# Kernel tuning notes

Hardware: AMD Instinct MI355X
Metric: run time of the kernel (lower is better)

The kernel has to match this reference:

```python
import jax, jax.numpy as jnp
import numpy as np

START_TAG = 30
END_TAG = 31
INVALID = -10000.0  # Constants.Invalid_Transition


def setup_inputs() -> dict:
    key = jax.random.key(0)
    k1, k2, k3, k4 = jax.random.split(key, 4)
    B, T, K = 1024, 512, 32
    feats = jax.random.normal(k1, (B, T, K), dtype=jnp.float32)
    tags = jax.random.randint(k2, (B, T), 0, START_TAG)  # gold tags exclude START/END
    lengths = jax.random.randint(k3, (B,), 1, T + 1)
    sentence_masks = (jnp.arange(T)[None, :] < lengths[:, None]).astype(jnp.int32)
    transitions = jax.random.normal(k4, (K, K), dtype=jnp.float32) * 0.1
    # transitions[i, j] = score of transitioning from tag j to tag i
    transitions = transitions.at[START_TAG, :].set(INVALID).at[:, END_TAG].set(INVALID)
    return {"feats": feats, "transitions": transitions, "tags": tags,
            "sentence_masks": sentence_masks}


def _gold_score(feats, transitions, tags, sentence_masks):
    # Faithful port of _score_sentence
    B, T, K = feats.shape
    emit = jnp.take_along_axis(feats, tags[:, :, None], axis=2)[:, :, 0]  # [B,T]
    emit = emit * sentence_masks.astype(feats.dtype)
    pad_start = jnp.concatenate([jnp.full((B, 1), START_TAG, tags.dtype), tags], axis=1)
    pad_end = jnp.concatenate([tags, jnp.full((B, 1), END_TAG, tags.dtype)], axis=1)
    trans = transitions[pad_end, pad_start]  # [B,T+1]
    tmask = jnp.concatenate([jnp.ones((B, 1), sentence_masks.dtype), sentence_masks], axis=1)
    trans = trans * tmask.astype(feats.dtype)
    return jnp.sum(emit, axis=1) + jnp.sum(trans, axis=1)  # [B]


def _log_partition(feats, transitions, sentence_masks):
    # Faithful port of _forward_alg: sequential DP over time, logsumexp over prev tags
    B, T, K = feats.shape
    lengths = jnp.sum(sentence_masks, axis=1)  # [B]
    init = jnp.full((K,), INVALID, dtype=feats.dtype).at[START_TAG].set(0.0)
    init = jnp.broadcast_to(init, (B, K))

    def step(forward_var, feat):
        # tag_var[b, next, prev] = alpha[b, prev] + trans[next, prev] + emit[b, next]
        tag_var = forward_var[:, None, :] + transitions[None, :, :] + feat[:, :, None]
        new = jax.nn.logsumexp(tag_var, axis=2)  # [B,K]
        return new, new

    _, all_alphas = jax.lax.scan(step, init, jnp.swapaxes(feats, 0, 1))  # [T,B,K]
    idx = jnp.broadcast_to((lengths - 1)[None, :, None], (1, B, K))
    last_alpha = jnp.take_along_axis(all_alphas, idx, axis=0)[0]  # [B,K]
    terminal = last_alpha + transitions[END_TAG][None, :]
    return jax.nn.logsumexp(terminal, axis=1)  # [B]


def reference(feats, transitions, tags, sentence_masks):
    # CRF negative log-likelihood per sentence: Z - gold_score
    Z = _log_partition(feats, transitions, sentence_masks)
    gold = _gold_score(feats, transitions, tags, sentence_masks)
    return Z - gold  # [B]
```

## Files before the change

### kernel.cpp

```cpp
#include <hip/hip_runtime.h>

#define KT 32
#define START_TAG 30
#define END_TAG 31

__device__ __forceinline__ float exp2f_fast(float x){ return __builtin_amdgcn_exp2f(x); }
__device__ __forceinline__ float log2f_fast(float x){ return __builtin_amdgcn_logf(x); }
__device__ __forceinline__ float readlane_f(float v, int l){
    return __int_as_float(__builtin_amdgcn_readlane(__float_as_int(v), l));
}

__global__ __launch_bounds__(128, 2) void crf_nll(
    const float* __restrict__ feats,
    const float* __restrict__ trans,
    const int*   __restrict__ tags,
    const int*   __restrict__ masks,
    float* __restrict__ out, int B, int T)
{
    constexpr float L2E = 1.4426950408889634f;
    constexpr float LN2 = 0.6931471805599453f;
    const int tid  = (int)threadIdx.x;
    const int lane = tid & 63;
    const int wid  = tid >> 6;
    const int k    = lane & 31;
    const int b    = (int)blockIdx.x;

    __shared__ float Tl[KT * KT];
    __shared__ __align__(16) float ftile[2][2][32][KT];
    __shared__ float cvec[KT];
    __shared__ int   cMF;

    for (int i = tid; i < KT * KT; i += 128) Tl[i] = trans[i];

    float E[KT];
    float E2 = 0.f;
    if (wid == 0) {
#pragma unroll
        for (int j = 0; j < KT; ++j) E[j] = exp2f_fast(trans[k * KT + j] * L2E);
    } else {
#pragma unroll
        for (int m = 0; m < KT; ++m) E[m] = exp2f_fast(trans[m * KT + k] * L2E);
        E2 = exp2f_fast(trans[END_TAG * KT + k] * L2E);
    }
    __syncthreads();

    const float4* f4 = (const float4*)(feats + (size_t)b * T * KT);
    const int*    mk = masks + (size_t)b * T;
    const int*    tg = tags  + (size_t)b * T;
    const float*  fb = feats + (size_t)b * T * KT;

    int Lp = 0;
    for (int c = 0; c < T; c += 64) { const int t = c + lane; if (t < T) Lp += mk[t]; }
#pragma unroll
    for (int d = 1; d < 64; d <<= 1) Lp += __shfl_xor(Lp, d);
    const int L   = Lp;
    const int mf  = (L + 1) >> 1;
    const int ntT = T >> 5;

    float4 R0, R1, R2, R3, S0, S1, S2, S3;
    float y = 0.f, Fc = 0.f, f1 = 0.f, f2 = 0.f, g = 0.f;
    int   M = 0;

#define TLOADR(ti_) { const int o=(ti_)*256+lane; R0=f4[o];R1=f4[o+64];R2=f4[o+128];R3=f4[o+192]; }
#define TLOADS(ti_) { const int o=(ti_)*256+lane; S0=f4[o];S1=f4[o+64];S2=f4[o+128];S3=f4[o+192]; }
#define TWRITER(bf) { float4* w=(float4*)&ftile[wid][bf][0][0]; w[lane]=R0;w[lane+64]=R1;w[lane+128]=R2;w[lane+192]=R3; }
#define TWRITES(bf) { float4* w=(float4*)&ftile[wid][bf][0][0]; w[lane]=S0;w[lane+64]=S1;w[lane+128]=S2;w[lane+192]=S3; }
#define FEAT(t_) ftile[wid][((t_)>>5)&1][(t_)&31][k]

    if (wid == 0) {
        TLOADR(0)
        if (ntT > 1) TLOADS(1)
        TWRITER(0)
        if (ntT > 1) TWRITES(1)
        y  = (k == START_TAG) ? 1.f : 0.f;
        Fc = exp2f_fast(FEAT(0) * L2E);
        f1 = FEAT(1);
        f2 = FEAT(2);
        const int ntA = (mf + 31) >> 5;
        for (int n = 0; n < ntA; ++n) {
            for (int c = 0; c < 4; ++c) {
#pragma unroll
                for (int u = 0; u < 8; ++u) {
                    const int ti_ = c * 8 + u;
                    const int t   = (n << 5) + ti_;
                    if (ti_ == 0)  { const int nx = n + 2; if (nx < ntA) TLOADR(nx) }
                    float sv[32];
#pragma unroll
                    for (int j = 0; j < 32; ++j) sv[j] = readlane_f(y, j);
                    __builtin_amdgcn_sched_barrier(0);
                    const unsigned pb = __float_as_uint(sv[0]);
                    int e = (int)((pb >> 23) & 255u);
                    if (e < 1 || e > 253) e = 127;
                    const float Fcr = Fc * __uint_as_float((unsigned)(254 - e) << 23);
                    float a0 = 0.f, a1 = 0.f, a2 = 0.f, a3 = 0.f;
#pragma unroll
                    for (int j = 0; j < 32; j += 4) {
                        a0 = fmaf(E[j+0], sv[j+0], a0);
                        a1 = fmaf(E[j+1], sv[j+1], a1);
                        a2 = fmaf(E[j+2], sv[j+2], a2);
                        a3 = fmaf(E[j+3], sv[j+3], a3);
                    }
                    const float val = ((a0 + a1) + (a2 + a3)) * Fcr;
                    const bool act = t < mf;
                    y  = act ? val : y;
                    M += act ? (e - 127) : 0;
                    if (ti_ == 30) { const int nx = n + 2; if (nx < ntA) TWRITER((n & 1)) }
                    const float fnew = FEAT(t + 3);
                    Fc = exp2f_fast(f1 * L2E);
                    f1 = f2; f2 = fnew;
                }
            }
        }
        if (lane < 32) cvec[k] = y;
        if (tid == 0) cMF = M;
    } else {
        const int n_hi = (L - 1) >> 5;
        const int n_lo = mf >> 5;
        TLOADR(n_hi)
        if (n_hi >= 1) TLOADS(n_hi - 1)
        float4 Q0, Q1, Q2, Q3;
        if (n_hi >= 2) { const int o=(n_hi-2)*256+lane; Q0=f4[o];Q1=f4[o+64];Q2=f4[o+128];Q3=f4[o+192]; }

        for (int c = 0; c < T; c += 64) {
            const int t = c + lane;
            if (t < T) {
                const int mt    = mk[t];
                const int tagt  = tg[t];
                const int prev  = t ? tg[t - 1] : START_TAG;
                const int fprev = t ? mk[t - 1] : 1;
                if (mt)    g += fb[(size_t)t * KT + tagt];
                if (fprev) g += Tl[tagt * KT + prev];
                if (t == T - 1 && mt) g += Tl[END_TAG * KT + tagt];
            }
        }
#pragma unroll
        for (int d = 1; d < 64; d <<= 1) g += __shfl_xor(g, d);

        TWRITER((n_hi & 1))
        if (n_hi >= 1) TWRITES(((n_hi - 1) & 1))
        y = E2; M = 0;
        Fc = exp2f_fast(FEAT(L - 1) * L2E);
        f1 = FEAT(L - 2);
        f2 = FEAT(L - 3);

#define BSTEP(T_, DO_LD, LD_TI, DO_WR, WR_BF) {                               \
        if (DO_LD) TLOADR(LD_TI)                                              \
        const float bb = y * Fc;                                              \
        float sv[32];                                                         \
        _Pragma("unroll")                                                     \
        for (int j = 0; j < 32; ++j) sv[j] = readlane_f(bb, j);               \
        __builtin_amdgcn_sched_barrier(0);                                    \
        const unsigned pb = __float_as_uint(sv[0]);                           \
        int e = (int)((pb >> 23) & 255u);                                     \
        if (e < 1 || e > 253) e = 127;                                        \
        const float r = __uint_as_float((unsigned)(254 - e) << 23);           \
        float a0 = 0.f, a1 = 0.f, a2 = 0.f, a3 = 0.f;                         \
        _Pragma("unroll")                                                     \
        for (int j = 0; j < 32; j += 4) {                                     \
            a0 = fmaf(E[j+0], sv[j+0], a0);                                   \
            a1 = fmaf(E[j+1], sv[j+1], a1);                                   \
            a2 = fmaf(E[j+2], sv[j+2], a2);                                   \
            a3 = fmaf(E[j+3], sv[j+3], a3);                                   \
        }                                                                     \
        const float val = ((a0 + a1) + (a2 + a3)) * r;                        \
        const bool act = (T_) >= mf;                                          \
        y  = act ? val : y;                                                   \
        M += act ? (e - 127) : 0;                                             \
        if (DO_WR) TWRITER(WR_BF)                                             \
        const float fnew = FEAT((T_) - 3);                                    \
        Fc = exp2f_fast(f1 * L2E);                                            \
        f1 = f2; f2 = fnew; }

        for (int t = L - 1; t >= (n_hi << 5); --t) {
            BSTEP(t, false, 0, false, 0)
        }
        if (n_hi >= 2) { float4* w=(float4*)&ftile[wid][(n_hi & 1)][0][0];
                         w[lane]=Q0;w[lane+64]=Q1;w[lane+128]=Q2;w[lane+192]=Q3; }
        for (int n = n_hi - 1; n >= n_lo; --n) {
            for (int c = 0; c < 4; ++c) {
#pragma unroll
                for (int u = 0; u < 8; ++u) {
                    const int ti_ = c * 8 + u;
                    const int t   = (n << 5) + 31 - ti_;
                    BSTEP(t, (ti_ == 0) && (n >= n_lo + 2), n - 2,
                             (ti_ == 29) && (n >= n_lo + 2), (n & 1))
                }
            }
        }
#undef BSTEP
    }

    __syncthreads();
    if (wid == 1) {
        float term = y * cvec[k];
#pragma unroll
        for (int d = 1; d < 32; d <<= 1) term += __shfl_xor(term, d);
        const float Z = ((float)(M + cMF) + log2f_fast(term)) * LN2;
        if (lane == 0) out[b] = Z - g;
    }
#undef TLOADR
#undef TLOADS
#undef TWRITER
#undef TWRITES
#undef FEAT
}

extern "C" void kernel_launch(void* const* d_in, const int* in_sizes, int n_in,
                              void* d_out, int out_size, void* d_ws, size_t ws_size,
                              hipStream_t stream) {
    const float* feats = (const float*)d_in[0];
    const float* trans = (const float*)d_in[1];
    const int*   tags  = (const int*)d_in[2];
    const int*   masks = (const int*)d_in[3];
    float* out = (float*)d_out;

    const int B = out_size;
    const int T = in_sizes[2] / B;

    hipLaunchKernelGGL(crf_nll, dim3(B), dim3(128), 0, stream,
                       feats, trans, tags, masks, out, B, T);
}
```

Measured before the change: 167.9 us.

## Split CRF matvec across wave halves using ds_swizzle broadcast

Each 32-lane half of the wavefront now handles 16 of the 32 previous tags, so a lane holds 16 transition exponentials instead of 32. The broadcasts use ds_swizzle in place of 32 serial readlanes, and the two partial sums are combined with a cross-half shuffle. The renormalization exponent is read with readfirstlane from the new state and applied at the next step, which takes the scale computation off the critical path. Swizzle and shuffle go through the LDS crossbar, which may add latency to each sequential step in place of the scalar readlane path.

New measurement: 152.8 us. -9.0%, faster.

```diff
diff --git a/kernel.cpp b/kernel.cpp
--- a/kernel.cpp
+++ b/kernel.cpp
@@ -6,9 +6,8 @@
 
 __device__ __forceinline__ float exp2f_fast(float x){ return __builtin_amdgcn_exp2f(x); }
 __device__ __forceinline__ float log2f_fast(float x){ return __builtin_amdgcn_logf(x); }
-__device__ __forceinline__ float readlane_f(float v, int l){
-    return __int_as_float(__builtin_amdgcn_readlane(__float_as_int(v), l));
-}
+
+#define SWZB(v, J) __int_as_float(__builtin_amdgcn_ds_swizzle(__float_as_int(v), ((J) << 5)))
 
 __global__ __launch_bounds__(128, 2) void crf_nll(
     const float* __restrict__ feats,
@@ -22,7 +21,9 @@
     const int tid  = (int)threadIdx.x;
     const int lane = tid & 63;
     const int wid  = tid >> 6;
-    const int k    = lane & 31;
+    const int li   = lane & 31;
+    const int h    = lane >> 5;
+    const int ok   = (li + (h << 4)) & 31;
     const int b    = (int)blockIdx.x;
 
     __shared__ float Tl[KT * KT];
@@ -32,15 +33,15 @@
 
     for (int i = tid; i < KT * KT; i += 128) Tl[i] = trans[i];
 
-    float E[KT];
-    float E2 = 0.f;
+    float Eh[16];
     if (wid == 0) {
 #pragma unroll
-        for (int j = 0; j < KT; ++j) E[j] = exp2f_fast(trans[k * KT + j] * L2E);
+        for (int j = 0; j < 16; ++j)
+            Eh[j] = exp2f_fast(trans[ok * KT + (h << 4) + j] * L2E);
     } else {
 #pragma unroll
-        for (int m = 0; m < KT; ++m) E[m] = exp2f_fast(trans[m * KT + k] * L2E);
-        E2 = exp2f_fast(trans[END_TAG * KT + k] * L2E);
+        for (int j = 0; j < 16; ++j)
+            Eh[j] = exp2f_fast(trans[((h << 4) + j) * KT + ok] * L2E);
     }
     __syncthreads();
 
@@ -53,30 +54,50 @@
     for (int c = 0; c < T; c += 64) { const int t = c + lane; if (t < T) Lp += mk[t]; }
 #pragma unroll
     for (int d = 1; d < 64; d <<= 1) Lp += __shfl_xor(Lp, d);
-    const int L   = Lp;
-    const int mf  = (L + 1) >> 1;
-    const int ntT = T >> 5;
+    const int L  = Lp;
+    const int mf = (L + 1) >> 1;
 
     float4 R0, R1, R2, R3, S0, S1, S2, S3;
-    float y = 0.f, Fc = 0.f, f1 = 0.f, f2 = 0.f, g = 0.f;
-    int   M = 0;
+    float y = 0.f, Fcr = 0.f, f1 = 0.f, f2 = 0.f, g = 0.f;
+    int   M = 0, dMp = 0;
 
 #define TLOADR(ti_) { const int o=(ti_)*256+lane; R0=f4[o];R1=f4[o+64];R2=f4[o+128];R3=f4[o+192]; }
 #define TLOADS(ti_) { const int o=(ti_)*256+lane; S0=f4[o];S1=f4[o+64];S2=f4[o+128];S3=f4[o+192]; }
 #define TWRITER(bf) { float4* w=(float4*)&ftile[wid][bf][0][0]; w[lane]=R0;w[lane+64]=R1;w[lane+128]=R2;w[lane+192]=R3; }
 #define TWRITES(bf) { float4* w=(float4*)&ftile[wid][bf][0][0]; w[lane]=S0;w[lane+64]=S1;w[lane+128]=S2;w[lane+192]=S3; }
-#define FEAT(t_) ftile[wid][((t_)>>5)&1][(t_)&31][k]
+#define FEAT(t_) ftile[wid][((t_)>>5)&1][(t_)&31][ok]
+
+#define MATVEC(SRC, SS)                                                        \
+    const float b0=SWZB(SRC,0),  b1=SWZB(SRC,1),  b2=SWZB(SRC,2),  b3=SWZB(SRC,3),  \
+                b4=SWZB(SRC,4),  b5=SWZB(SRC,5),  b6=SWZB(SRC,6),  b7=SWZB(SRC,7),  \
+                b8=SWZB(SRC,8),  b9=SWZB(SRC,9),  b10=SWZB(SRC,10),b11=SWZB(SRC,11),\
+                b12=SWZB(SRC,12),b13=SWZB(SRC,13),b14=SWZB(SRC,14),b15=SWZB(SRC,15);\
+    float a0 = Eh[0]*b0, a1 = Eh[1]*b1, a2 = Eh[2]*b2, a3 = Eh[3]*b3;          \
+    a0 = fmaf(Eh[4], b4, a0);  a1 = fmaf(Eh[5], b5, a1);                       \
+    a2 = fmaf(Eh[6], b6, a2);  a3 = fmaf(Eh[7], b7, a3);                       \
+    a0 = fmaf(Eh[8], b8, a0);  a1 = fmaf(Eh[9], b9, a1);                       \
+    a2 = fmaf(Eh[10],b10,a2);  a3 = fmaf(Eh[11],b11,a3);                       \
+    a0 = fmaf(Eh[12],b12,a0);  a1 = fmaf(Eh[13],b13,a1);                       \
+    a2 = fmaf(Eh[14],b14,a2);  a3 = fmaf(Eh[15],b15,a3);                       \
+    const float pp = (a0 + a1) + (a2 + a3);                                    \
+    const float SS = pp + __shfl_xor(pp, 48);
+
+#define CAPTURE(SS)                                                            \
+    { const int cap = __builtin_amdgcn_readfirstlane(__float_as_int(SS));      \
+      int e = (cap >> 23) & 255; if (e < 1 || e > 253) e = 127;                \
+      dMp = e - 127;                                                           \
+      Fcr = exp2f_fast(f1 * L2E) * __uint_as_float((unsigned)(254 - e) << 23); }
 
     if (wid == 0) {
+        const int ntA = (mf + 31) >> 5;
         TLOADR(0)
-        if (ntT > 1) TLOADS(1)
+        if (ntA > 1) TLOADS(1)
         TWRITER(0)
-        if (ntT > 1) TWRITES(1)
-        y  = (k == START_TAG) ? 1.f : 0.f;
-        Fc = exp2f_fast(FEAT(0) * L2E);
-        f1 = FEAT(1);
-        f2 = FEAT(2);
-        const int ntA = (mf + 31) >> 5;
+        if (ntA > 1) TWRITES(1)
+        y   = (ok == START_TAG) ? 1.f : 0.f;
+        Fcr = exp2f_fast(FEAT(0) * L2E);
+        f1  = FEAT(1);
+        f2  = FEAT(2);
         for (int n = 0; n < ntA; ++n) {
             for (int c = 0; c < 4; ++c) {
 #pragma unroll
@@ -84,35 +105,20 @@
                     const int ti_ = c * 8 + u;
                     const int t   = (n << 5) + ti_;
                     if (ti_ == 0)  { const int nx = n + 2; if (nx < ntA) TLOADR(nx) }
-                    float sv[32];
-#pragma unroll
-                    for (int j = 0; j < 32; ++j) sv[j] = readlane_f(y, j);
-                    __builtin_amdgcn_sched_barrier(0);
-                    const unsigned pb = __float_as_uint(sv[0]);
-                    int e = (int)((pb >> 23) & 255u);
-                    if (e < 1 || e > 253) e = 127;
-                    const float Fcr = Fc * __uint_as_float((unsigned)(254 - e) << 23);
-                    float a0 = 0.f, a1 = 0.f, a2 = 0.f, a3 = 0.f;
-#pragma unroll
-                    for (int j = 0; j < 32; j += 4) {
-                        a0 = fmaf(E[j+0], sv[j+0], a0);
-                        a1 = fmaf(E[j+1], sv[j+1], a1);
-                        a2 = fmaf(E[j+2], sv[j+2], a2);
-                        a3 = fmaf(E[j+3], sv[j+3], a3);
-                    }
-                    const float val = ((a0 + a1) + (a2 + a3)) * Fcr;
-                    const bool act = t < mf;
+                    const float fnew = FEAT(t + 3);
+                    MATVEC(y, ss)
+                    const float val = ss * Fcr;
+                    const bool  act = t < mf;
                     y  = act ? val : y;
-                    M += act ? (e - 127) : 0;
+                    M += act ? dMp : 0;
+                    CAPTURE(ss)
                     if (ti_ == 30) { const int nx = n + 2; if (nx < ntA) TWRITER((n & 1)) }
-                    const float fnew = FEAT(t + 3);
-                    Fc = exp2f_fast(f1 * L2E);
                     f1 = f2; f2 = fnew;
                 }
             }
         }
-        if (lane < 32) cvec[k] = y;
-        if (tid == 0) cMF = M;
+        if (lane < 32) cvec[lane] = y;
+        if (tid == 0)  cMF = M;
     } else {
         const int n_hi = (L - 1) >> 5;
         const int n_lo = mf >> 5;
@@ -138,37 +144,21 @@
 
         TWRITER((n_hi & 1))
         if (n_hi >= 1) TWRITES(((n_hi - 1) & 1))
-        y = E2; M = 0;
-        Fc = exp2f_fast(FEAT(L - 1) * L2E);
-        f1 = FEAT(L - 2);
-        f2 = FEAT(L - 3);
+        y   = exp2f_fast(trans[END_TAG * KT + ok] * L2E);
+        Fcr = exp2f_fast(FEAT(L - 1) * L2E);
+        f1  = FEAT(L - 2);
+        f2  = FEAT(L - 3);
 
 #define BSTEP(T_, DO_LD, LD_TI, DO_WR, WR_BF) {                               \
         if (DO_LD) TLOADR(LD_TI)                                              \
-        const float bb = y * Fc;                                              \
-        float sv[32];                                                         \
-        _Pragma("unroll")                                                     \
-        for (int j = 0; j < 32; ++j) sv[j] = readlane_f(bb, j);               \
-        __builtin_amdgcn_sched_barrier(0);                                    \
-        const unsigned pb = __float_as_uint(sv[0]);                           \
-        int e = (int)((pb >> 23) & 255u);                                     \
-        if (e < 1 || e > 253) e = 127;                                        \
-        const float r = __uint_as_float((unsigned)(254 - e) << 23);           \
-        float a0 = 0.f, a1 = 0.f, a2 = 0.f, a3 = 0.f;                         \
-        _Pragma("unroll")                                                     \
-        for (int j = 0; j < 32; j += 4) {                                     \
-            a0 = fmaf(E[j+0], sv[j+0], a0);                                   \
-            a1 = fmaf(E[j+1], sv[j+1], a1);                                   \
-            a2 = fmaf(E[j+2], sv[j+2], a2);                                   \
-            a3 = fmaf(E[j+3], sv[j+3], a3);                                   \
-        }                                                                     \
-        const float val = ((a0 + a1) + (a2 + a3)) * r;                        \
+        const float fnew = FEAT((T_) - 3);                                    \
+        const float bb = y * Fcr;                                             \
+        MATVEC(bb, ss)                                                        \
         const bool act = (T_) >= mf;                                          \
-        y  = act ? val : y;                                                   \
-        M += act ? (e - 127) : 0;                                             \
+        y  = act ? ss : y;                                                    \
+        M += act ? dMp : 0;                                                   \
+        CAPTURE(ss)                                                           \
         if (DO_WR) TWRITER(WR_BF)                                             \
-        const float fnew = FEAT((T_) - 3);                                    \
-        Fc = exp2f_fast(f1 * L2E);                                            \
         f1 = f2; f2 = fnew; }
 
         for (int t = L - 1; t >= (n_hi << 5); --t) {
@@ -192,10 +182,10 @@
 
     __syncthreads();
     if (wid == 1) {
-        float term = y * cvec[k];
-#pragma unroll
-        for (int d = 1; d < 32; d <<= 1) term += __shfl_xor(term, d);
-        const float Z = ((float)(M + cMF) + log2f_fast(term)) * LN2;
+        float term = y * cvec[ok];
+#pragma unroll
+        for (int d = 1; d < 64; d <<= 1) term += __shfl_xor(term, d);
+        const float Z = ((float)(M + cMF) + log2f_fast(term * 0.5f)) * LN2;
         if (lane == 0) out[b] = Z - g;
     }
 #undef TLOADR
@@ -203,6 +193,8 @@
 #undef TWRITER
 #undef TWRITES
 #undef FEAT
+#undef MATVEC
+#undef CAPTURE
 }
 
 extern "C" void kernel_launch(void* const* d_in, const int* in_sizes, int n_in,
```
